# Performance work log

Hardware: AMD Instinct MI355X
Metric: run time of the kernel (lower is better)

The kernel has to match this reference:

```python
import jax, jax.numpy as jnp
import numpy as np

EPS = 1e-5

def _bin_act(x):
    # sign() forward, clipped straight-through estimator backward
    xc = jnp.clip(x, -1.0, 1.0)
    return xc + jax.lax.stop_gradient(jnp.sign(x) - xc)

def _bin_w(w):
    # XNOR-style: sign(w) scaled by per-output-channel mean(|w|); identity STE
    alpha = jnp.mean(jnp.abs(w), axis=(1, 2, 3), keepdims=True)
    return w + jax.lax.stop_gradient(jnp.sign(w) * alpha - w)

def _conv(x, w, stride, padding, groups):
    return jax.lax.conv_general_dilated(
        x, w, window_strides=(stride, stride),
        padding=[(padding, padding), (padding, padding)],
        feature_group_count=groups,
        dimension_numbers=('NCHW', 'OIHW', 'NCHW'))

def _binconv(x, w, stride, padding, groups):
    return _conv(_bin_act(x), _bin_w(w), stride, padding, groups)

def _bn(x, g, b, m, v):
    # eval-mode BatchNorm2d
    inv = g / jnp.sqrt(v + EPS)
    return x * inv[None, :, None, None] + (b - m * inv)[None, :, None, None]


def setup_inputs() -> dict:
    key = jax.random.key(0)
    ks = jax.random.split(key, 20)
    inp, oup = 256, 512
    d = {}
    d['x'] = jax.random.normal(ks[0], (64, inp, 28, 28), jnp.float32)
    d['w1'] = jax.random.normal(ks[1], (inp, 16, 3, 3), jnp.float32) * 0.1  # grouped, groups=inp/16
    d['w2'] = jax.random.normal(ks[2], (oup, inp, 1, 1), jnp.float32) * 0.05
    d['w3'] = jax.random.normal(ks[3], (oup, oup, 1, 1), jnp.float32) * 0.05
    for i, (name, c) in enumerate([('1', inp), ('2', oup), ('3', oup)]):
        d['g' + name] = jax.random.uniform(ks[4 + 4 * i], (c,), jnp.float32, 0.5, 1.5)
        d['b' + name] = jax.random.normal(ks[5 + 4 * i], (c,), jnp.float32) * 0.1
        d['m' + name] = jax.random.normal(ks[6 + 4 * i], (c,), jnp.float32) * 0.1
        d['v' + name] = jax.random.uniform(ks[7 + 4 * i], (c,), jnp.float32, 0.5, 1.5)
    return d


def reference(x, w1, w2, w3, g1, b1, m1, v1, g2, b2, m2, v2, g3, b3, m3, v3):
    inp = x.shape[1]
    groups = inp // 16
    # conv1 (binary grouped 3x3) + bn1 + residual + hardtanh
    out = _bn(_binconv(x, w1, 1, 1, groups), g1, b1, m1, v1)
    out = jnp.clip(out + x, -1.0, 1.0)
    # conv2 (binary 1x1, inp->oup) + bn2 + hardtanh
    out = jnp.clip(_bn(_binconv(out, w2, 1, 0, 1), g2, b2, m2, v2), -1.0, 1.0)
    res = out
    # conv3 (binary 1x1, oup->oup) + bn3 + residual + hardtanh
    out = _bn(_binconv(out, w3, 1, 0, 1), g3, b3, m3, v3)
    return jnp.clip(out + res, -1.0, 1.0)
```

## Files before the change

kernel.cpp:

```cpp
#include <hip/hip_runtime.h>
#include <stdint.h>

#define C1 256
#define C2 512
#define P_ 784
#define TAU 1e-6

typedef int v4i __attribute__((ext_vector_type(4)));

#define WS_NEED 2071104

#define K23_SMEM 69632

__global__ __launch_bounds__(256) void prep(
    const float* __restrict__ w1, const float* __restrict__ w2, const float* __restrict__ w3,
    const float* __restrict__ g1, const float* __restrict__ b1, const float* __restrict__ m1, const float* __restrict__ v1,
    const float* __restrict__ g2, const float* __restrict__ b2, const float* __restrict__ m2, const float* __restrict__ v2,
    const float* __restrict__ g3, const float* __restrict__ b3, const float* __restrict__ m3, const float* __restrict__ v3,
    double* __restrict__ sc1d, double* __restrict__ bi1d,
    int* __restrict__ T2, float* __restrict__ sc2f, float* __restrict__ bi2f,
    float* __restrict__ sc3f, float* __restrict__ bi3f,
    uint16_t* __restrict__ wb1, uint32_t* __restrict__ w2i8w, uint32_t* __restrict__ w3i8w,
    int* __restrict__ rs2, int* __restrict__ rs3,
    unsigned long long* __restrict__ amin)
{
    int bid = blockIdx.x, t = threadIdx.x;
    if (bid == 0 && t == 0) amin[0] = ~0ULL;
    if (bid == 0) {
        int co = t;
        const float* wp = w1 + (size_t)co * 144;
        double s = 0.0;
        for (int k = 0; k < 144; k++) s += fabs((double)wp[k]);
        double alpha = s / 144.0;
        double iv = (double)g1[co] / sqrt((double)v1[co] + 1e-5);
        sc1d[co] = alpha * iv;
        bi1d[co] = (double)b1[co] - (double)m1[co] * iv;
        for (int tap = 0; tap < 9; tap++) {
            uint32_t wv = 0;
            for (int ci = 0; ci < 16; ci++) wv |= (uint32_t)(wp[ci * 9 + tap] < 0.f) << ci;
            wb1[co * 9 + tap] = (uint16_t)wv;
        }
    } else if (bid <= 2) {
        int co = (bid - 1) * 256 + t;
        const float* wp = w2 + (size_t)co * 256;
        double s = 0.0;
        for (int k = 0; k < 256; k++) s += fabs((double)wp[k]);
        double alpha = s / 256.0;
        double iv = (double)g2[co] / sqrt((double)v2[co] + 1e-5);
        double sc = alpha * iv;
        double bi = (double)b2[co] - (double)m2[co] * iv;
        int T = -257;
        while (T <= 257 && fma((double)T, sc, bi) < 0.0) T++;
        T2[co] = T;
        sc2f[co] = (float)sc;
        bi2f[co] = (float)bi;
        int neg = 0;
        for (int wd = 0; wd < 64; wd++) {
            uint32_t b4 = 0;
            for (int j = 0; j < 4; j++) {
                int sbit = (wp[wd * 4 + j] < 0.f);
                neg += sbit;
                b4 |= (sbit ? 0xFFu : 0x01u) << (8 * j);
            }
            w2i8w[co * 64 + wd] = b4;
        }
        rs2[co] = 256 - 2 * neg;
    } else {
        int co = (bid - 3) * 256 + t;
        const float* wp = w3 + (size_t)co * 512;
        double s = 0.0;
        for (int k = 0; k < 512; k++) s += fabs((double)wp[k]);
        double alpha = s / 512.0;
        double iv = (double)g3[co] / sqrt((double)v3[co] + 1e-5);
        sc3f[co] = (float)(alpha * iv);
        bi3f[co] = (float)((double)b3[co] - (double)m3[co] * iv);
        int neg = 0;
        for (int wd = 0; wd < 128; wd++) {
            uint32_t b4 = 0;
            for (int j = 0; j < 4; j++) {
                int sbit = (wp[wd * 4 + j] < 0.f);
                neg += sbit;
                b4 |= (sbit ? 0xFFu : 0x01u) << (8 * j);
            }
            w3i8w[co * 128 + wd] = b4;
        }
        rs3[co] = 512 - 2 * neg;
    }
}

__global__ __launch_bounds__(256) void k1(
    const float* __restrict__ x,
    const double* __restrict__ sc1d, const double* __restrict__ bi1d,
    const uint16_t* __restrict__ wb1,
    uint16_t* __restrict__ pk1, unsigned long long* __restrict__ amin)
{
    __shared__ uint32_t xzb[30][30];
    __shared__ uint16_t wbl[16][9];
    __shared__ double scs[16], bis[16];
    __shared__ float scf[16], bif[16];

    int g = blockIdx.x, n = blockIdx.y, t = threadIdx.x;

    for (int idx = t; idx < 900; idx += 256) ((uint32_t*)xzb)[idx] = 0;
    if (t < 144) ((uint16_t*)wbl)[t] = wb1[g * 144 + t];
    if (t < 16) {
        scs[t] = sc1d[g * 16 + t]; bis[t] = bi1d[g * 16 + t];
        scf[t] = (float)scs[t];    bif[t] = (float)bis[t];
    }
    __syncthreads();

    const float* xg = x + ((size_t)n * C1 + g * 16) * P_;
    float xr[4][16];
    #pragma unroll
    for (int i = 0; i < 4; i++) {
        int p = t + 256 * i;
        if (p < P_) {
            uint32_t sb = 0, nb = 0;
            #pragma unroll
            for (int ci = 0; ci < 16; ci++) {
                float xv = xg[ci * P_ + p];
                xr[i][ci] = xv;
                sb |= (uint32_t)(xv < 0.f) << ci;
                nb |= (uint32_t)(xv != 0.f) << ci;
            }
            int h = p / 28, w = p - 28 * h;
            xzb[h + 1][w + 1] = sb | (nb << 16);
        }
    }
    __syncthreads();

    uint16_t* pko = pk1 + ((size_t)n * 16 + g) * P_;
    #pragma unroll
    for (int i = 0; i < 4; i++) {
        int p = t + 256 * i;
        if (p < P_) {
            int h = p / 28, w = p - 28 * h;
            uint32_t xv9[9], zv9[9];
            int Z = 0;
            #pragma unroll
            for (int kh = 0; kh < 3; kh++)
                #pragma unroll
                for (int kw = 0; kw < 3; kw++) {
                    int k = kh * 3 + kw;
                    uint32_t xz = xzb[h + kh][w + kw];
                    xv9[k] = xz & 0xFFFFu;
                    zv9[k] = xz >> 16;
                    Z += __popc(zv9[k]);
                }
            uint32_t word = 0;
            #pragma unroll
            for (int co = 0; co < 16; co++) {
                int pd = 0;
                #pragma unroll
                for (int k = 0; k < 9; k++)
                    pd += __popc((xv9[k] ^ (uint32_t)wbl[co][k]) & zv9[k]);
                int S = Z - 2 * pd;
                float vf = __fmaf_rn((float)S, scf[co], bif[co]) + xr[i][co];
                uint32_t neg;
                if (fabsf(vf) < 1e-3f) {
                    double v = fma((double)S, scs[co], bis[co]) + (double)xr[i][co];
                    v = fmin(fmax(v, -1.0), 1.0);
                    double m = fabs(v);
                    if (m < TAU) {
                        unsigned long long pk =
                            ((unsigned long long)__float_as_uint((float)m) << 32) |
                            (unsigned long long)((uint32_t)(n * C1 + g * 16 + co) * (uint32_t)P_ + (uint32_t)p);
                        atomicMin(amin, pk);
                    }
                    neg = (v < 0.0);
                } else {
                    neg = (vf < 0.f);
                }
                word |= neg << co;
            }
            pko[p] = (uint16_t)word;
        }
    }
}

__global__ __launch_bounds__(512, 4) void k23m(
    const uint8_t* __restrict__ w2i8, const uint8_t* __restrict__ w3i8,
    const int* __restrict__ rs2g, const int* __restrict__ rs3g,
    const int* __restrict__ T2g,
    const float* __restrict__ sc2f, const float* __restrict__ bi2f,
    const float* __restrict__ sc3f, const float* __restrict__ bi3f,
    const uint16_t* __restrict__ pk1, const unsigned long long* __restrict__ amin,
    float* __restrict__ out)
{
    extern __shared__ char smem[];
    char*  s1Tb = smem;
    char*  B2Tb = smem + 17408;
    float* stg  = (float*)(smem + 51200);

    int n = blockIdx.x, pc = blockIdx.y, t = threadIdx.x;
    int w = t >> 6, l = t & 63;
    int lm = l & 15, lh = l >> 4, klo = lh * 16;
    int p0 = 64 * pc;
    int UN = (pc == 12) ? 16 : 64;
    int NPT = UN / 16;
    float* stagef = stg + w * 576;

    const uint32_t* pkw = (const uint32_t*)(pk1 + (size_t)n * 16 * P_);
    int UNW = UN / 2;
    for (int idx = t; idx < 16 * UNW; idx += 512) {
        int g = idx / UNW, jj = idx % UNW;
        uint32_t wpair = pkw[g * 392 + 32 * pc + jj];
        #pragma unroll
        for (int hf = 0; hf < 2; hf++) {
            uint32_t w16 = (wpair >> (16 * hf)) & 0xFFFFu;
            int row = 2 * jj + hf;
            #pragma unroll
            for (int q = 0; q < 4; q++) {
                uint32_t nib = (w16 >> (4 * q)) & 0xFu;
                uint32_t v = (nib & 1u) | ((nib & 2u) << 7) | ((nib & 4u) << 14) | ((nib & 8u) << 21);
                *(uint32_t*)(s1Tb + row * 272 + g * 16 + q * 4) = v;
            }
        }
    }
    __syncthreads();
    if (t == 0) {
        unsigned long long a = amin[0];
        if (a != ~0ULL) {
            uint32_t loc = (uint32_t)a;
            uint32_t nn = loc / (C1 * P_);
            uint32_t rem = loc - nn * C1 * P_;
            uint32_t c = rem / P_;
            int p = (int)(rem - c * P_);
            if ((int)nn == n && p >= p0 && p < p0 + UN)
                s1Tb[(p - p0) * 272 + c] ^= 1;
        }
    }
    __syncthreads();

    for (int j = 0; j < 4; j++) {
        int co0 = 64 * w + 16 * j;
        int rs2v[4], T2v[4];
        #pragma unroll
        for (int r = 0; r < 4; r++) {
            int cr = co0 + lh * 4 + r;
            rs2v[r] = rs2g[cr]; T2v[r] = T2g[cr];
        }
        v4i a1[4];
        #pragma unroll
        for (int ks = 0; ks < 4; ks++)
            a1[ks] = *(const v4i*)(w2i8 + (size_t)(co0 + lm) * 256 + ks * 64 + klo);
        for (int pt = 0; pt < NPT; pt++) {
            const char* bp = s1Tb + (pt * 16 + lm) * 272;
            v4i acc = {0, 0, 0, 0};
            #pragma unroll
            for (int ks = 0; ks < 4; ks++) {
                v4i b = *(const v4i*)(bp + ks * 64 + klo);
                acc = __builtin_amdgcn_mfma_i32_16x16x64_i8(a1[ks], b, acc, 0, 0, 0);
            }
            int rowb = (pt * 16 + lm) * 528;
            #pragma unroll
            for (int r = 0; r < 4; r++) {
                int S2 = rs2v[r] - 2 * acc[r];
                B2Tb[rowb + co0 + lh * 4 + r] = (char)(S2 < T2v[r]);
            }
        }
    }
    __syncthreads();

    for (int j2 = 0; j2 < 4; j2++) {
        int co0 = 64 * w + 16 * j2;
        int rs2v[4], rs3v[4];
        float sc2v[4], bi2v[4], sc3v[4], bi3v[4];
        #pragma unroll
        for (int r = 0; r < 4; r++) {
            int cr = co0 + lh * 4 + r;
            rs2v[r] = rs2g[cr]; sc2v[r] = sc2f[cr]; bi2v[r] = bi2f[cr];
            rs3v[r] = rs3g[cr]; sc3v[r] = sc3f[cr]; bi3v[r] = bi3f[cr];
        }
        v4i a1[4];
        #pragma unroll
        for (int ks = 0; ks < 4; ks++)
            a1[ks] = *(const v4i*)(w2i8 + (size_t)(co0 + lm) * 256 + ks * 64 + klo);
        v4i a3[8];
        #pragma unroll
        for (int ks = 0; ks < 8; ks++)
            a3[ks] = *(const v4i*)(w3i8 + (size_t)(co0 + lm) * 512 + ks * 64 + klo);

        for (int pt = 0; pt < NPT; pt++) {
            const char* bp = s1Tb + (pt * 16 + lm) * 272;
            v4i acc1 = {0, 0, 0, 0};
            #pragma unroll
            for (int ks = 0; ks < 4; ks++) {
                v4i b = *(const v4i*)(bp + ks * 64 + klo);
                acc1 = __builtin_amdgcn_mfma_i32_16x16x64_i8(a1[ks], b, acc1, 0, 0, 0);
            }
            float r2[4];
            #pragma unroll
            for (int r = 0; r < 4; r++) {
                int S2 = rs2v[r] - 2 * acc1[r];
                r2[r] = fminf(fmaxf(__fmaf_rn((float)S2, sc2v[r], bi2v[r]), -1.f), 1.f);
            }
            const char* bp2 = B2Tb + (pt * 16 + lm) * 528;
            v4i acc3 = {0, 0, 0, 0};
            #pragma unroll
            for (int ks = 0; ks < 8; ks++) {
                v4i b = *(const v4i*)(bp2 + ks * 64 + klo);
                acc3 = __builtin_amdgcn_mfma_i32_16x16x64_i8(a3[ks], b, acc3, 0, 0, 0);
            }
            #pragma unroll
            for (int r = 0; r < 4; r++) {
                int S3 = rs3v[r] - 2 * acc3[r];
                float v = __fmaf_rn((float)S3, sc3v[r], bi3v[r]) + r2[r];
                v = fminf(fmaxf(v, -1.f), 1.f);
                stagef[(lh * 4 + r) * 36 + (pt & 1) * 16 + lm] = v;
            }
            if ((pt & 1) == 1 || pt == NPT - 1) {
                asm volatile("s_waitcnt lgkmcnt(0)" ::: "memory");
                int pb = p0 + (pt & ~1) * 16;
                int ncols = (pt & 1) ? 32 : 16;
                int col = (l & 7) * 4;
                #pragma unroll
                for (int g2 = 0; g2 < 2; g2++) {
                    if (col < ncols) {
                        int cc = co0 + g2 * 8 + (l >> 3);
                        float4 val = *(float4*)(stagef + (g2 * 8 + (l >> 3)) * 36 + col);
                        *(float4*)(out + ((size_t)n * C2 + cc) * P_ + pb + col) = val;
                    }
                }
            }
        }
    }
}

extern "C" void kernel_launch(void* const* d_in, const int* in_sizes, int n_in,
                              void* d_out, int out_size, void* d_ws, size_t ws_size,
                              hipStream_t stream) {
    const float* x  = (const float*)d_in[0];
    const float* w1 = (const float*)d_in[1];
    const float* w2 = (const float*)d_in[2];
    const float* w3 = (const float*)d_in[3];
    const float* g1 = (const float*)d_in[4];
    const float* b1 = (const float*)d_in[5];
    const float* m1 = (const float*)d_in[6];
    const float* v1 = (const float*)d_in[7];
    const float* g2 = (const float*)d_in[8];
    const float* b2 = (const float*)d_in[9];
    const float* m2 = (const float*)d_in[10];
    const float* v2 = (const float*)d_in[11];
    const float* g3 = (const float*)d_in[12];
    const float* b3 = (const float*)d_in[13];
    const float* m3 = (const float*)d_in[14];
    const float* v3 = (const float*)d_in[15];
    float* out = (float*)d_out;

    char* ws = (char*)d_ws;
    unsigned long long* amin = (unsigned long long*)(ws + 0);
    double*   sc1d = (double*)(ws + 64);
    double*   bi1d = (double*)(ws + 2112);
    int*      T2   = (int*)(ws + 4160);
    float*    sc2f = (float*)(ws + 6208);
    float*    bi2f = (float*)(ws + 8256);
    float*    sc3f = (float*)(ws + 10304);
    float*    bi3f = (float*)(ws + 12352);
    uint16_t* wb1  = (uint16_t*)(ws + 14400);
    uint16_t* pk1  = (uint16_t*)(ws + 68160);
    uint8_t*  w2i8 = (uint8_t*)(ws + 1673792);
    uint8_t*  w3i8 = (uint8_t*)(ws + 1804864);
    int*      rs2  = (int*)(ws + 2067008);
    int*      rs3  = (int*)(ws + 2069056);

    prep<<<dim3(5), 256, 0, stream>>>(w1, w2, w3,
        g1, b1, m1, v1, g2, b2, m2, v2, g3, b3, m3, v3,
        sc1d, bi1d, T2, sc2f, bi2f, sc3f, bi3f, wb1,
        (uint32_t*)w2i8, (uint32_t*)w3i8, rs2, rs3, amin);
    k1<<<dim3(16, 64), 256, 0, stream>>>(x, sc1d, bi1d, wb1, pk1, amin);
    k23m<<<dim3(64, 13), 512, K23_SMEM, stream>>>(w2i8, w3i8, rs2, rs3, T2,
        sc2f, bi2f, sc3f, bi3f, pk1, amin, out);
}
```

Baseline: 140.4 us.

## Shrink k23m tiles to 32 pixels with 256 threads for more blocks

The fused conv2/conv3 kernel now processes 32 pixel columns per block with 256 threads, where it used 64 columns with 512. This gives 25 pixel chunks per image instead of 13, so more blocks can spread across CUs, and shared memory use drops. The packed bits are first staged raw in LDS, where the near-zero flip is applied, and then unpacked cooperatively; this replaces the strided global-load unpack. Each block now reloads the full w2/w3 weight fragments for fewer pixels, which raises weight traffic per output.

New measurement: 186.1 us. 32.6% more time.

```diff
diff --git a/kernel.cpp b/kernel.cpp
--- a/kernel.cpp
+++ b/kernel.cpp
@@ -10,7 +10,7 @@
 
 #define WS_NEED 2071104
 
-#define K23_SMEM 69632
+#define K23_SMEM 35904
 
 __global__ __launch_bounds__(256) void prep(
     const float* __restrict__ w1, const float* __restrict__ w2, const float* __restrict__ w3,
@@ -178,7 +178,7 @@
     }
 }
 
-__global__ __launch_bounds__(512, 4) void k23m(
+__global__ __launch_bounds__(256, 4) void k23m(
     const uint8_t* __restrict__ w2i8, const uint8_t* __restrict__ w3i8,
     const int* __restrict__ rs2g, const int* __restrict__ rs3g,
     const int* __restrict__ T2g,
@@ -188,34 +188,23 @@
     float* __restrict__ out)
 {
     extern __shared__ char smem[];
-    char*  s1Tb = smem;
-    char*  B2Tb = smem + 17408;
-    float* stg  = (float*)(smem + 51200);
+    uint16_t* raws = (uint16_t*)smem;
+    char*  s1Tb = smem + 1088;
+    char*  B2Tb = smem + 9792;
+    float* stg  = (float*)(smem + 26688);
 
     int n = blockIdx.x, pc = blockIdx.y, t = threadIdx.x;
     int w = t >> 6, l = t & 63;
     int lm = l & 15, lh = l >> 4, klo = lh * 16;
-    int p0 = 64 * pc;
-    int UN = (pc == 12) ? 16 : 64;
-    int NPT = UN / 16;
+    int p0 = 32 * pc;
     float* stagef = stg + w * 576;
 
     const uint32_t* pkw = (const uint32_t*)(pk1 + (size_t)n * 16 * P_);
-    int UNW = UN / 2;
-    for (int idx = t; idx < 16 * UNW; idx += 512) {
-        int g = idx / UNW, jj = idx % UNW;
-        uint32_t wpair = pkw[g * 392 + 32 * pc + jj];
-        #pragma unroll
-        for (int hf = 0; hf < 2; hf++) {
-            uint32_t w16 = (wpair >> (16 * hf)) & 0xFFFFu;
-            int row = 2 * jj + hf;
-            #pragma unroll
-            for (int q = 0; q < 4; q++) {
-                uint32_t nib = (w16 >> (4 * q)) & 0xFu;
-                uint32_t v = (nib & 1u) | ((nib & 2u) << 7) | ((nib & 4u) << 14) | ((nib & 8u) << 21);
-                *(uint32_t*)(s1Tb + row * 272 + g * 16 + q * 4) = v;
-            }
-        }
+    {
+        uint32_t* raw32 = (uint32_t*)raws;
+        int g = t >> 4, jj = t & 15;
+        int src = 16 * pc + jj;
+        raw32[g * 17 + jj] = (src < 392) ? pkw[g * 392 + src] : 0u;
     }
     __syncthreads();
     if (t == 0) {
@@ -226,14 +215,25 @@
             uint32_t rem = loc - nn * C1 * P_;
             uint32_t c = rem / P_;
             int p = (int)(rem - c * P_);
-            if ((int)nn == n && p >= p0 && p < p0 + UN)
-                s1Tb[(p - p0) * 272 + c] ^= 1;
-        }
-    }
-    __syncthreads();
-
-    for (int j = 0; j < 4; j++) {
-        int co0 = 64 * w + 16 * j;
+            if ((int)nn == n && p >= p0 && p < p0 + 32)
+                raws[(c >> 4) * 34 + (p - p0)] ^= (uint16_t)(1u << (c & 15));
+        }
+    }
+    __syncthreads();
+    #pragma unroll
+    for (int k = 0; k < 8; k++) {
+        int idx = t + 256 * k;
+        int row = idx >> 6, c4 = idx & 63;
+        uint32_t w16 = raws[(c4 >> 2) * 34 + row];
+        uint32_t nib = (w16 >> (4 * (c4 & 3))) & 0xFu;
+        uint32_t v = (nib & 1u) | ((nib & 2u) << 7) | ((nib & 4u) << 14) | ((nib & 8u) << 21);
+        *(uint32_t*)(s1Tb + row * 272 + c4 * 4) = v;
+    }
+    __syncthreads();
+
+    #pragma unroll 1
+    for (int j = 0; j < 8; j++) {
+        int co0 = 128 * w + 16 * j;
         int rs2v[4], T2v[4];
         #pragma unroll
         for (int r = 0; r < 4; r++) {
@@ -244,7 +244,8 @@
         #pragma unroll
         for (int ks = 0; ks < 4; ks++)
             a1[ks] = *(const v4i*)(w2i8 + (size_t)(co0 + lm) * 256 + ks * 64 + klo);
-        for (int pt = 0; pt < NPT; pt++) {
+        #pragma unroll
+        for (int pt = 0; pt < 2; pt++) {
             const char* bp = s1Tb + (pt * 16 + lm) * 272;
             v4i acc = {0, 0, 0, 0};
             #pragma unroll
@@ -262,8 +263,9 @@
     }
     __syncthreads();
 
-    for (int j2 = 0; j2 < 4; j2++) {
-        int co0 = 64 * w + 16 * j2;
+    #pragma unroll 1
+    for (int j2 = 0; j2 < 8; j2++) {
+        int co0 = 128 * w + 16 * j2;
         int rs2v[4], rs3v[4];
         float sc2v[4], bi2v[4], sc3v[4], bi3v[4];
         #pragma unroll
@@ -281,7 +283,8 @@
         for (int ks = 0; ks < 8; ks++)
             a3[ks] = *(const v4i*)(w3i8 + (size_t)(co0 + lm) * 512 + ks * 64 + klo);
 
-        for (int pt = 0; pt < NPT; pt++) {
+        #pragma unroll
+        for (int pt = 0; pt < 2; pt++) {
             const char* bp = s1Tb + (pt * 16 + lm) * 272;
             v4i acc1 = {0, 0, 0, 0};
             #pragma unroll
@@ -307,20 +310,18 @@
                 int S3 = rs3v[r] - 2 * acc3[r];
                 float v = __fmaf_rn((float)S3, sc3v[r], bi3v[r]) + r2[r];
                 v = fminf(fmaxf(v, -1.f), 1.f);
-                stagef[(lh * 4 + r) * 36 + (pt & 1) * 16 + lm] = v;
-            }
-            if ((pt & 1) == 1 || pt == NPT - 1) {
-                asm volatile("s_waitcnt lgkmcnt(0)" ::: "memory");
-                int pb = p0 + (pt & ~1) * 16;
-                int ncols = (pt & 1) ? 32 : 16;
-                int col = (l & 7) * 4;
-                #pragma unroll
-                for (int g2 = 0; g2 < 2; g2++) {
-                    if (col < ncols) {
-                        int cc = co0 + g2 * 8 + (l >> 3);
-                        float4 val = *(float4*)(stagef + (g2 * 8 + (l >> 3)) * 36 + col);
-                        *(float4*)(out + ((size_t)n * C2 + cc) * P_ + pb + col) = val;
-                    }
+                stagef[(lh * 4 + r) * 36 + pt * 16 + lm] = v;
+            }
+        }
+        asm volatile("s_waitcnt lgkmcnt(0)" ::: "memory");
+        {
+            int col = (l & 7) * 4;
+            #pragma unroll
+            for (int g2 = 0; g2 < 2; g2++) {
+                if (p0 + col + 4 <= P_) {
+                    int cc = co0 + g2 * 8 + (l >> 3);
+                    float4 val = *(float4*)(stagef + (g2 * 8 + (l >> 3)) * 36 + col);
+                    *(float4*)(out + ((size_t)n * C2 + cc) * P_ + p0 + col) = val;
                 }
             }
         }
@@ -369,6 +370,6 @@
         sc1d, bi1d, T2, sc2f, bi2f, sc3f, bi3f, wb1,
         (uint32_t*)w2i8, (uint32_t*)w3i8, rs2, rs3, amin);
     k1<<<dim3(16, 64), 256, 0, stream>>>(x, sc1d, bi1d, wb1, pk1, amin);
-    k23m<<<dim3(64, 13), 512, K23_SMEM, stream>>>(w2i8, w3i8, rs2, rs3, T2,
+    k23m<<<dim3(64, 25), 256, K23_SMEM, stream>>>(w2i8, w3i8, rs2, rs3, T2,
         sc2f, bi2f, sc3f, bi3f, pk1, amin, out);
 }
```
